# Optimization experiments

Hardware: AMD Instinct MI355X
Metric: run time of the kernel (lower is better)

The kernel has to match this reference:

```python
import jax, jax.numpy as jnp
import numpy as np

B, H, S, D = 4, 16, 2048, 64


def setup_inputs() -> dict:
    key = jax.random.key(0)
    kq, kk, kv = jax.random.split(key, 3)
    Q = jax.random.normal(kq, (B, H, S, D), dtype=jnp.float32)
    K = jax.random.normal(kk, (B, H, S, D), dtype=jnp.float32)
    V = jax.random.normal(kv, (B, H, S, D), dtype=jnp.float32)
    # causal mask, broadcasts over (B, H); True = keep, False (==0) = mask out
    mask = jnp.tril(jnp.ones((S, S), dtype=bool))
    return {"Q": Q, "K": K, "V": V, "mask": mask}


def reference(Q, K, V, mask):
    d_k = Q.shape[-1]
    scale = 1.0 / jnp.sqrt(jnp.asarray(d_k, dtype=Q.dtype))
    # [B,H,Sq,Sk] score matrix (the module materializes this fully)
    scores = jnp.einsum('bhqd,bhkd->bhqk', Q, K) * scale
    if mask is not None:
        scores = jnp.where(mask, scores, -jnp.inf)
    attn = jax.nn.softmax(scores, axis=-1)
    return jnp.einsum('bhqk,bhkd->bhqd', attn, V)
```

## Files before the change

### kernel.cpp

```cpp
#include <hip/hip_runtime.h>
#include <math.h>

namespace {

constexpr int SEQ   = 2048;
constexpr int DH    = 64;
constexpr int KVBLK = 64;
constexpr int QW    = 32;
constexpr int NWAVE = 4;
constexpr int QBLK  = QW * NWAVE;
constexpr int NQB   = SEQ / QBLK;
constexpr int BH    = 64;
constexpr int PADB  = 72;

typedef __bf16 bf16x8 __attribute__((ext_vector_type(8)));
typedef float  f32x16 __attribute__((ext_vector_type(16)));

union FragB { bf16x8 v; unsigned u[4]; __bf16 h[8]; };

__device__ __forceinline__ unsigned pack2(float a, float b) {
  union { __bf16 h[2]; unsigned u; } x;
  x.h[0] = (__bf16)a; x.h[1] = (__bf16)b;
  return x.u;
}

__device__ __forceinline__ void swap32(int a, int b, int &x, int &y) {
#if __has_builtin(__builtin_amdgcn_permlane32_swap)
  auto r = __builtin_amdgcn_permlane32_swap(a, b, false, false);
  x = r[0]; y = r[1];
#else
  const bool hi = ((threadIdx.x & 63) >= 32);
  const int sa = __shfl_xor(a, 32), sb = __shfl_xor(b, 32);
  x = hi ? sb : a;
  y = hi ? b  : sa;
#endif
}

__device__ __forceinline__ float xhalf_sum(float v) {
  int x, y; swap32(__float_as_int(v), __float_as_int(v), x, y);
  return __int_as_float(x) + __int_as_float(y);
}

__global__ __launch_bounds__(256, 2)
void attn_fwd(const float* __restrict__ Qg, const float* __restrict__ Kg,
              const float* __restrict__ Vg, float* __restrict__ Og)
{
  const int b   = blockIdx.x;
  const int xcd = b & 7;
  const int idx = b >> 3;
  const int qi  = (NQB - 1) - (idx >> 3);
  const int bh  = xcd + 8 * (idx & 7);
  const int qb  = qi * QBLK;
  const int qb64 = qb >> 6;

  const int tid  = threadIdx.x;
  const int wv   = tid >> 6;
  const int lane = tid & 63;
  const int l31  = lane & 31;
  const int hi   = lane >> 5;

  const size_t base = (size_t)bh * SEQ * DH;
  const float* Qp = Qg + base;
  const float* Kp = Kg + base;
  const float* Vp = Vg + base;
  float*       Op = Og + base;

  __shared__ __align__(16) unsigned char smem[36864];
  auto K_lds  = reinterpret_cast<__bf16(*)[KVBLK][PADB]>(smem);
  auto Vt_lds = reinterpret_cast<__bf16(*)[DH][PADB]>(smem + 18432);

  const float qscale = 0.125f * 1.44269504088896f;
  FragB bq[4];
  const int wq0 = wv * QW;
  {
    const float* src = Qp + (size_t)(qb + wq0 + l31) * DH + hi*8;
#pragma unroll
    for (int ks = 0; ks < 4; ++ks) {
      float4 f0 = *(const float4*)(src + ks*16);
      float4 f1 = *(const float4*)(src + ks*16 + 4);
      FragB f;
      f.h[0]=(__bf16)(f0.x*qscale); f.h[1]=(__bf16)(f0.y*qscale);
      f.h[2]=(__bf16)(f0.z*qscale); f.h[3]=(__bf16)(f0.w*qscale);
      f.h[4]=(__bf16)(f1.x*qscale); f.h[5]=(__bf16)(f1.y*qscale);
      f.h[6]=(__bf16)(f1.z*qscale); f.h[7]=(__bf16)(f1.w*qscale);
      bq[ks] = f;
    }
  }

  float4 kr[2][2];
  float  vr[16];
  const int kc8 = tid & 7;
  const int vd  = tid & 63;
  const int vk0 = (tid >> 6) * 16;

  auto load_tile = [&](int t) {
    const int kvb = t * KVBLK;
#pragma unroll
    for (int p = 0; p < 2; ++p) {
      const float* s = Kp + (size_t)(kvb + 32*p + (tid >> 3)) * DH + kc8*8;
      kr[p][0] = *(const float4*)s;
      kr[p][1] = *(const float4*)(s + 4);
    }
#pragma unroll
    for (int r = 0; r < 16; ++r)
      vr[r] = Vp[(size_t)(kvb + vk0 + r) * DH + vd];
  };

  auto store_tile = [&](int buf) {
#pragma unroll
    for (int p = 0; p < 2; ++p) {
      uint4 w;
      w.x = pack2(kr[p][0].x, kr[p][0].y); w.y = pack2(kr[p][0].z, kr[p][0].w);
      w.z = pack2(kr[p][1].x, kr[p][1].y); w.w = pack2(kr[p][1].z, kr[p][1].w);
      *reinterpret_cast<uint4*>(&K_lds[buf][32*p + (tid >> 3)][kc8*8]) = w;
    }
    uint4 w0, w1;
    w0.x = pack2(vr[0],  vr[1]);  w0.y = pack2(vr[2],  vr[3]);
    w0.z = pack2(vr[4],  vr[5]);  w0.w = pack2(vr[6],  vr[7]);
    w1.x = pack2(vr[8],  vr[9]);  w1.y = pack2(vr[10], vr[11]);
    w1.z = pack2(vr[12], vr[13]); w1.w = pack2(vr[14], vr[15]);
    *reinterpret_cast<uint4*>(&Vt_lds[buf][vd][vk0])     = w0;
    *reinterpret_cast<uint4*>(&Vt_lds[buf][vd][vk0 + 8]) = w1;
  };

  f32x16 oacc[2];
#pragma unroll
  for (int dt = 0; dt < 2; ++dt)
#pragma unroll
    for (int r = 0; r < 16; ++r) oacc[dt][r] = 0.f;
  float lpart = 0.f;

  const int NT = qb64 + 2;
  const int tmax_wave = qb64 + (wv >> 1);
  const int qloc = (wv & 1) * 32 + l31;

  load_tile(0);
  store_tile(0);
  __syncthreads();

  for (int t = 0; t < NT; ++t) {
    const int cur = t & 1;
    if (t + 1 < NT) load_tile(t + 1);

    if (t <= tmax_wave) {
      const bool diag = (t == tmax_wave);

      f32x16 st[2];
#pragma unroll
      for (int T = 0; T < 2; ++T)
#pragma unroll
        for (int r = 0; r < 16; ++r) st[T][r] = 0.f;
      __builtin_amdgcn_s_setprio(1);
#pragma unroll
      for (int T = 0; T < 2; ++T)
#pragma unroll
        for (int ks = 0; ks < 4; ++ks) {
          bf16x8 ak = *(const bf16x8*)&K_lds[cur][T*32 + l31][ks*16 + hi*8];
          st[T] = __builtin_amdgcn_mfma_f32_32x32x16_bf16(ak, bq[ks].v, st[T], 0, 0, 0);
        }
      __builtin_amdgcn_s_setprio(0);

      float p[2][16];
#pragma unroll
      for (int T = 0; T < 2; ++T)
#pragma unroll
        for (int r = 0; r < 16; ++r) {
          float s = st[T][r];
          if (diag) {
            const int kvl = T*32 + (r & 3) + 4*hi + 8*(r >> 2);
            if (kvl > qloc) s = -INFINITY;
          }
          const float e = exp2f(s);
          p[T][r] = e;
          lpart += e;
        }

      unsigned pk[2][8];
#pragma unroll
      for (int T = 0; T < 2; ++T)
#pragma unroll
        for (int j = 0; j < 8; ++j) pk[T][j] = pack2(p[T][2*j], p[T][2*j + 1]);

      FragB pa[4];
#pragma unroll
      for (int ks = 0; ks < 4; ++ks) {
        const int T  = ks >> 1;
        const int gA = (2*ks) & 3;
        const int gB = (2*ks + 1) & 3;
        int x0, y0, x1, y1;
        swap32((int)pk[T][2*gA],     (int)pk[T][2*gB],     x0, y0);
        swap32((int)pk[T][2*gA + 1], (int)pk[T][2*gB + 1], x1, y1);
        pa[ks].u[0] = (unsigned)x0;
        pa[ks].u[1] = (unsigned)x1;
        pa[ks].u[2] = (unsigned)y0;
        pa[ks].u[3] = (unsigned)y1;
      }

      __builtin_amdgcn_s_setprio(1);
#pragma unroll
      for (int dt = 0; dt < 2; ++dt)
#pragma unroll
        for (int ks = 0; ks < 4; ++ks) {
          bf16x8 av = *(const bf16x8*)&Vt_lds[cur][dt*32 + l31][ks*16 + hi*8];
          oacc[dt] = __builtin_amdgcn_mfma_f32_32x32x16_bf16(av, pa[ks].v, oacc[dt], 0, 0, 0);
        }
      __builtin_amdgcn_s_setprio(0);
    }

    if (t + 1 < NT) store_tile(cur ^ 1);
    __syncthreads();
  }

  const float linv = 1.0f / xhalf_sum(lpart);
  float* slab = reinterpret_cast<float*>(smem) + wv * (QW * 68);

#pragma unroll
  for (int dt = 0; dt < 2; ++dt)
#pragma unroll
    for (int g = 0; g < 4; ++g) {
      float4 w;
      w.x = oacc[dt][4*g + 0] * linv;
      w.y = oacc[dt][4*g + 1] * linv;
      w.z = oacc[dt][4*g + 2] * linv;
      w.w = oacc[dt][4*g + 3] * linv;
      *(float4*)&slab[l31*68 + dt*32 + 8*g + 4*hi] = w;
    }
  __syncthreads();
  {
    float* dst = Op + (size_t)(qb + wq0) * DH;
#pragma unroll
    for (int i = 0; i < 8; ++i) {
      const int row = i*4 + (lane >> 4);
      const int ch  = lane & 15;
      float4 v = *(const float4*)&slab[row*68 + ch*4];
      *(float4*)&dst[(size_t)row*DH + ch*4] = v;
    }
  }
}

}

extern "C" void kernel_launch(void* const* d_in, const int* in_sizes, int n_in,
                              void* d_out, int out_size, void* d_ws, size_t ws_size,
                              hipStream_t stream) {
  const float* Q = (const float*)d_in[0];
  const float* K = (const float*)d_in[1];
  const float* V = (const float*)d_in[2];
  float* O = (float*)d_out;
  attn_fwd<<<dim3(NQB * BH), dim3(256), 0, stream>>>(Q, K, V, O);
}
```

Baseline: 84.17 us.

## Pair complementary causal query blocks in one 512-thread block sharing K/V tiles

Each 512-thread block now handles two 128-row query blocks, a late one (15-p) and an early one (p). Waves 0-3 and 4-7 share the same K/V tiles staged in LDS, so global K/V loads and bf16 conversion happen once per tile for both halves. Block indices are also mapped so a heavy and a light pairing tend to run together and the same head stays on one XCD. The trade-off is that the early half's waves sit idle at barriers once their causal range is done, and the epilogue takes two rounds to reuse the LDS slab.

```diff
diff --git a/kernel.cpp b/kernel.cpp
--- a/kernel.cpp
+++ b/kernel.cpp
@@ -7,8 +7,7 @@
 constexpr int DH    = 64;
 constexpr int KVBLK = 64;
 constexpr int QW    = 32;
-constexpr int NWAVE = 4;
-constexpr int QBLK  = QW * NWAVE;
+constexpr int QBLK  = 128;
 constexpr int NQB   = SEQ / QBLK;
 constexpr int BH    = 64;
 constexpr int PADB  = 72;
@@ -41,23 +40,31 @@
   return __int_as_float(x) + __int_as_float(y);
 }
 
-__global__ __launch_bounds__(256, 2)
+__global__ __launch_bounds__(512, 2)
 void attn_fwd(const float* __restrict__ Qg, const float* __restrict__ Kg,
               const float* __restrict__ Vg, float* __restrict__ Og)
 {
-  const int b   = blockIdx.x;
-  const int xcd = b & 7;
-  const int idx = b >> 3;
-  const int qi  = (NQB - 1) - (idx >> 3);
-  const int bh  = xcd + 8 * (idx & 7);
-  const int qb  = qi * QBLK;
-  const int qb64 = qb >> 6;
+  const int b    = blockIdx.x;
+  const int half = b >> 8;
+  const int r_   = b & 255;
+  const int bh   = r_ & 63;
+  const int pu   = r_ >> 6;
+  const int p    = half ? (7 - pu) : pu;
+  const int qiA  = 15 - p;
 
   const int tid  = threadIdx.x;
   const int wv   = tid >> 6;
+  const int wvl  = wv & 3;
+  const bool isA = (wv < 4);
   const int lane = tid & 63;
   const int l31  = lane & 31;
   const int hi   = lane >> 5;
+
+  const int qi_w = isA ? qiA : p;
+  const int qb_w = qi_w * QBLK + wvl * QW;
+  const int NT   = 2 * qiA + 2;
+  const int tmax_wave = 2 * qi_w + (wvl >> 1);
+  const int qloc = (wvl & 1) * 32 + l31;
 
   const size_t base = (size_t)bh * SEQ * DH;
   const float* Qp = Qg + base;
@@ -71,9 +78,8 @@
 
   const float qscale = 0.125f * 1.44269504088896f;
   FragB bq[4];
-  const int wq0 = wv * QW;
   {
-    const float* src = Qp + (size_t)(qb + wq0 + l31) * DH + hi*8;
+    const float* src = Qp + (size_t)(qb_w + l31) * DH + hi*8;
 #pragma unroll
     for (int ks = 0; ks < 4; ++ks) {
       float4 f0 = *(const float4*)(src + ks*16);
@@ -87,40 +93,32 @@
     }
   }
 
-  float4 kr[2][2];
-  float  vr[16];
-  const int kc8 = tid & 7;
-  const int vd  = tid & 63;
-  const int vk0 = (tid >> 6) * 16;
+  float4 kr0, kr1;
+  float  vr[8];
+  const int krow = tid >> 3;
+  const int kc8  = tid & 7;
+  const int vd   = tid & 63;
+  const int vk0  = wv * 8;
 
   auto load_tile = [&](int t) {
     const int kvb = t * KVBLK;
-#pragma unroll
-    for (int p = 0; p < 2; ++p) {
-      const float* s = Kp + (size_t)(kvb + 32*p + (tid >> 3)) * DH + kc8*8;
-      kr[p][0] = *(const float4*)s;
-      kr[p][1] = *(const float4*)(s + 4);
-    }
-#pragma unroll
-    for (int r = 0; r < 16; ++r)
+    const float* s = Kp + (size_t)(kvb + krow) * DH + kc8*8;
+    kr0 = *(const float4*)s;
+    kr1 = *(const float4*)(s + 4);
+#pragma unroll
+    for (int r = 0; r < 8; ++r)
       vr[r] = Vp[(size_t)(kvb + vk0 + r) * DH + vd];
   };
 
   auto store_tile = [&](int buf) {
-#pragma unroll
-    for (int p = 0; p < 2; ++p) {
-      uint4 w;
-      w.x = pack2(kr[p][0].x, kr[p][0].y); w.y = pack2(kr[p][0].z, kr[p][0].w);
-      w.z = pack2(kr[p][1].x, kr[p][1].y); w.w = pack2(kr[p][1].z, kr[p][1].w);
-      *reinterpret_cast<uint4*>(&K_lds[buf][32*p + (tid >> 3)][kc8*8]) = w;
-    }
-    uint4 w0, w1;
-    w0.x = pack2(vr[0],  vr[1]);  w0.y = pack2(vr[2],  vr[3]);
-    w0.z = pack2(vr[4],  vr[5]);  w0.w = pack2(vr[6],  vr[7]);
-    w1.x = pack2(vr[8],  vr[9]);  w1.y = pack2(vr[10], vr[11]);
-    w1.z = pack2(vr[12], vr[13]); w1.w = pack2(vr[14], vr[15]);
-    *reinterpret_cast<uint4*>(&Vt_lds[buf][vd][vk0])     = w0;
-    *reinterpret_cast<uint4*>(&Vt_lds[buf][vd][vk0 + 8]) = w1;
+    uint4 wk;
+    wk.x = pack2(kr0.x, kr0.y); wk.y = pack2(kr0.z, kr0.w);
+    wk.z = pack2(kr1.x, kr1.y); wk.w = pack2(kr1.z, kr1.w);
+    *reinterpret_cast<uint4*>(&K_lds[buf][krow][kc8*8]) = wk;
+    uint4 wv4;
+    wv4.x = pack2(vr[0], vr[1]); wv4.y = pack2(vr[2], vr[3]);
+    wv4.z = pack2(vr[4], vr[5]); wv4.w = pack2(vr[6], vr[7]);
+    *reinterpret_cast<uint4*>(&Vt_lds[buf][vd][vk0]) = wv4;
   };
 
   f32x16 oacc[2];
@@ -129,10 +127,6 @@
 #pragma unroll
     for (int r = 0; r < 16; ++r) oacc[dt][r] = 0.f;
   float lpart = 0.f;
-
-  const int NT = qb64 + 2;
-  const int tmax_wave = qb64 + (wv >> 1);
-  const int qloc = (wv & 1) * 32 + l31;
 
   load_tile(0);
   store_tile(0);
@@ -160,7 +154,7 @@
         }
       __builtin_amdgcn_s_setprio(0);
 
-      float p[2][16];
+      float pv[2][16];
 #pragma unroll
       for (int T = 0; T < 2; ++T)
 #pragma unroll
@@ -171,7 +165,7 @@
             if (kvl > qloc) s = -INFINITY;
           }
           const float e = exp2f(s);
-          p[T][r] = e;
+          pv[T][r] = e;
           lpart += e;
         }
 
@@ -179,7 +173,7 @@
 #pragma unroll
       for (int T = 0; T < 2; ++T)
 #pragma unroll
-        for (int j = 0; j < 8; ++j) pk[T][j] = pack2(p[T][2*j], p[T][2*j + 1]);
+        for (int j = 0; j < 8; ++j) pk[T][j] = pack2(pv[T][2*j], pv[T][2*j + 1]);
 
       FragB pa[4];
 #pragma unroll
@@ -212,28 +206,34 @@
   }
 
   const float linv = 1.0f / xhalf_sum(lpart);
-  float* slab = reinterpret_cast<float*>(smem) + wv * (QW * 68);
-
-#pragma unroll
-  for (int dt = 0; dt < 2; ++dt)
-#pragma unroll
-    for (int g = 0; g < 4; ++g) {
-      float4 w;
-      w.x = oacc[dt][4*g + 0] * linv;
-      w.y = oacc[dt][4*g + 1] * linv;
-      w.z = oacc[dt][4*g + 2] * linv;
-      w.w = oacc[dt][4*g + 3] * linv;
-      *(float4*)&slab[l31*68 + dt*32 + 8*g + 4*hi] = w;
-    }
-  __syncthreads();
-  {
-    float* dst = Op + (size_t)(qb + wq0) * DH;
-#pragma unroll
-    for (int i = 0; i < 8; ++i) {
-      const int row = i*4 + (lane >> 4);
-      const int ch  = lane & 15;
-      float4 v = *(const float4*)&slab[row*68 + ch*4];
-      *(float4*)&dst[(size_t)row*DH + ch*4] = v;
+  float* slab = reinterpret_cast<float*>(smem) + (wv & 3) * (QW * 68);
+
+#pragma unroll
+  for (int round = 0; round < 2; ++round) {
+    __syncthreads();
+    if ((wv >> 2) == round) {
+#pragma unroll
+      for (int dt = 0; dt < 2; ++dt)
+#pragma unroll
+        for (int g = 0; g < 4; ++g) {
+          float4 w;
+          w.x = oacc[dt][4*g + 0] * linv;
+          w.y = oacc[dt][4*g + 1] * linv;
+          w.z = oacc[dt][4*g + 2] * linv;
+          w.w = oacc[dt][4*g + 3] * linv;
+          *(float4*)&slab[l31*68 + dt*32 + 8*g + 4*hi] = w;
+        }
+    }
+    __syncthreads();
+    if ((wv >> 2) == round) {
+      float* dst = Op + (size_t)qb_w * DH;
+#pragma unroll
+      for (int i = 0; i < 8; ++i) {
+        const int row = i*4 + (lane >> 4);
+        const int ch  = lane & 15;
+        float4 v = *(const float4*)&slab[row*68 + ch*4];
+        *(float4*)&dst[(size_t)row*DH + ch*4] = v;
+      }
     }
   }
 }
@@ -247,5 +247,5 @@
   const float* K = (const float*)d_in[1];
   const float* V = (const float*)d_in[2];
   float* O = (float*)d_out;
-  attn_fwd<<<dim3(NQB * BH), dim3(256), 0, stream>>>(Q, K, V, O);
-}
+  attn_fwd<<<dim3(BH * 8), dim3(512), 0, stream>>>(Q, K, V, O);
+}
```

New measurement: 100.9 us. 19.9% more time.
